# Kernel tuning notes

Hardware: AMD Instinct MI355X
Metric: run time of the kernel (lower is better)

The kernel has to match this reference:

```python
import jax, jax.numpy as jnp
import numpy as np

D_K = 64


def setup_inputs() -> dict:
    key = jax.random.key(0)
    kq, kk, kv, km = jax.random.split(key, 4)
    B, H, S = 4, 16, 2048
    Q = jax.random.normal(kq, (B, H, S, D_K), dtype=jnp.float32)
    K = jax.random.normal(kk, (B, H, S, D_K), dtype=jnp.float32)
    V = jax.random.normal(kv, (B, H, S, D_K), dtype=jnp.float32)
    # boolean mask, True = masked out; broadcast over heads
    mask = jax.random.randint(km, (B, 1, S, S), 0, 2).astype(jnp.bool_)
    return {"Q": Q, "K": K, "V": V, "mask": mask}


def reference(Q, K, V, mask):
    scale = jnp.sqrt(jnp.asarray(D_K, dtype=Q.dtype))
    # [B,H,S,S] scores
    scores = jnp.einsum('bhqd,bhkd->bhqk', Q, K) / scale
    scores = jnp.where(mask, jnp.asarray(-1e9, dtype=scores.dtype), scores)
    attn = jax.nn.softmax(scores, axis=-1)
    return jnp.einsum('bhqk,bhkd->bhqd', attn, V)
```

## Files before the change

### kernel.cpp

```cpp
#include <hip/hip_runtime.h>
#include <hip/hip_bf16.h>


#define SEQ   2048
#define DK    64
#define NB_   4
#define NBH   64
#define KVB   64
#define QB    128
#define NT    (SEQ / KVB)

#define MASKH_WORDS ((size_t)NB_ * SEQ * 64)
#define WSK_OFF ((size_t)2 * 1024 * 1024)
#define WSV_OFF ((size_t)18 * 1024 * 1024)
#define WS_NEED ((size_t)34 * 1024 * 1024)

typedef float    f32x16 __attribute__((ext_vector_type(16)));
typedef _Float16 f16x8  __attribute__((ext_vector_type(8)));
typedef _Float16 f16x2v __attribute__((ext_vector_type(2)));

#define QSCALE 0.18033688011112042f

#if __has_builtin(__builtin_amdgcn_exp2f)
#define EXP2F(x) __builtin_amdgcn_exp2f(x)
#else
__device__ __forceinline__ float EXP2F(float x) {
  float r;
  asm("v_exp_f32 %0, %1\n\ts_nop 1" : "=v"(r) : "v"(x));
  return r;
}
#endif

__device__ __forceinline__ unsigned pkrtz(float lo, float hi) {
  auto v = __builtin_amdgcn_cvt_pkrtz(lo, hi);
  return __builtin_bit_cast(unsigned, v);
}

__device__ __forceinline__ float mzero(float v, unsigned mw, int idx) {
  int s = ((int)(mw << (31 - idx))) >> 31;
  unsigned r = __builtin_bit_cast(unsigned, v) & ~(unsigned)s;
  return __builtin_bit_cast(float, r);
}

#define GLOAD16(g, l)                                                          \
  __builtin_amdgcn_global_load_lds(                                            \
      (const __attribute__((address_space(1))) unsigned*)(g),                  \
      (__attribute__((address_space(3))) unsigned*)(l), 16, 0, 0)

#define BARRIER()                                          \
  do {                                                     \
    asm volatile("s_waitcnt lgkmcnt(0)" ::: "memory");     \
    __builtin_amdgcn_s_barrier();                          \
  } while (0)

__device__ __forceinline__ void halfswap(unsigned a, unsigned b,
                                         unsigned& out_lo, unsigned& out_hi, int hiL) {
#if __has_builtin(__builtin_amdgcn_permlane32_swap)
  auto r = __builtin_amdgcn_permlane32_swap(a, b, false, false);
  out_lo = r[0];
  out_hi = r[1];
#else
  unsigned ax = __shfl_xor(a, 32), bx = __shfl_xor(b, 32);
  out_lo = hiL ? bx : a;
  out_hi = hiL ? b : ax;
#endif
}

__global__ __launch_bounds__(256) void pre_all(
    const int* __restrict__ M, const float* __restrict__ K,
    const float* __restrict__ V, unsigned* __restrict__ Mh,
    _Float16* __restrict__ wsK, _Float16* __restrict__ wsV) {
  const int blk = blockIdx.x;
  if (blk < 2048) {
    int t  = blk * 256 + threadIdx.x;
    int hi = t & 1, T = (t >> 1) & 31, q = (t >> 6) & 2047, b = t >> 17;
    const int* src = M + ((size_t)b * SEQ + q) * SEQ + T * 64 + 4 * hi;
    unsigned bits = 0;
#pragma unroll
    for (int kvb = 0; kvb < 2; ++kvb)
#pragma unroll
      for (int m = 0; m < 4; ++m) {
        int4 v = *(const int4*)(src + 32 * kvb + 8 * m);
        int sh = 16 * kvb + 4 * m;
        bits |= ((unsigned)(v.x != 0) << sh) | ((unsigned)(v.y != 0) << (sh + 1)) |
                ((unsigned)(v.z != 0) << (sh + 2)) | ((unsigned)(v.w != 0) << (sh + 3));
      }
    Mh[t] = bits;
  } else if (blk < 6144) {
    int t  = (blk - 2048) * 256 + threadIdx.x;
    int lq = t & 31, c = (t >> 5) & 15, kt = (t >> 9) & 31, bh = t >> 14;
    int kv = kt * 64 + (c >> 3) * 32 + lq;
    int d0 = ((c >> 1) & 3) * 16 + (c & 1) * 8;
    const float4* src = (const float4*)(K + ((size_t)bh * SEQ + kv) * DK + d0);
    float4 a = src[0], b4 = src[1];
    uint4 o = { pkrtz(a.x, a.y), pkrtz(a.z, a.w), pkrtz(b4.x, b4.y), pkrtz(b4.z, b4.w) };
    *(uint4*)(wsK + (size_t)t * 8) = o;
  } else {
    int t  = (blk - 6144) * 256 + threadIdx.x;
    int lq = t & 31, c = (t >> 5) & 15, kt = (t >> 9) & 31, bh = t >> 14;
    int kv0 = kt * 64 + ((c >> 1) & 3) * 16 + (c & 1) * 8;
    int d   = (c >> 3) * 32 + lq;
    const float* vp = V + ((size_t)bh * SEQ + kv0) * DK + d;
    float v[8];
#pragma unroll
    for (int j = 0; j < 8; ++j) v[j] = vp[(size_t)j * DK];
    uint4 o = { pkrtz(v[0], v[1]), pkrtz(v[2], v[3]), pkrtz(v[4], v[5]), pkrtz(v[6], v[7]) };
    *(uint4*)(wsV + (size_t)t * 8) = o;
  }
}


__global__ __launch_bounds__(256) void sda_attn_pc(
    const float* __restrict__ Q, const unsigned* __restrict__ Mh,
    const _Float16* __restrict__ wsK, const _Float16* __restrict__ wsV,
    float* __restrict__ O) {
  __shared__ __align__(16) _Float16 Kl[2][16 * 256];
  __shared__ __align__(16) _Float16 Vt[3][16 * 256];

  const int bh   = blockIdx.x;
  const int qt   = blockIdx.y;
  const int b    = bh >> 4;
  const int tid  = threadIdx.x;
  const int wid  = tid >> 6;
  const int lane = tid & 63;
  const int lq   = lane & 31;
  const int hiL  = lane >> 5;

  const size_t base = (size_t)bh * SEQ * DK;
  const int    q    = qt * QB + wid * 32 + lq;

  f16x8 qf[4];
  {
    const float* qp = Q + base + (size_t)q * DK + hiL * 8;
#pragma unroll
    for (int kk = 0; kk < 4; ++kk) {
      float4 A  = *(const float4*)(qp + kk * 16);
      float4 Bv = *(const float4*)(qp + kk * 16 + 4);
      uint4 u;
      u.x = pkrtz(A.x * QSCALE, A.y * QSCALE);
      u.y = pkrtz(A.z * QSCALE, A.w * QSCALE);
      u.z = pkrtz(Bv.x * QSCALE, Bv.y * QSCALE);
      u.w = pkrtz(Bv.z * QSCALE, Bv.w * QSCALE);
      qf[kk] = __builtin_bit_cast(f16x8, u);
    }
  }

  f32x16 oacc[2];
#pragma unroll
  for (int db = 0; db < 2; ++db)
#pragma unroll
    for (int r = 0; r < 16; ++r) oacc[db][r] = 0.f;
  float lreg = 0.f;

  const _Float16* skb = wsK + (size_t)bh * 32 * 4096 + wid * 1024 + lane * 8;
  const _Float16* svb = wsV + (size_t)bh * 32 * 4096 + wid * 1024 + lane * 8;
  const unsigned* Mhp = Mh + ((size_t)b * SEQ + q) * 64 + hiL;
  const f16x2v ones = {(_Float16)1.0f, (_Float16)1.0f};
  (void)ones;

#define STAGE2(j_)                                            \
  {                                                           \
    const _Float16* sk = skb + (size_t)(j_) * 4096;           \
    const _Float16* sv = svb + (size_t)(j_) * 4096;           \
    _Float16* dk = &Kl[(j_) & 1][wid * 1024];                 \
    _Float16* dv = &Vt[(j_) % 3][wid * 1024];                 \
    GLOAD16(sk, dk); GLOAD16(sk + 512, dk + 512);             \
    GLOAD16(sv, dv); GLOAD16(sv + 512, dv + 512);             \
  }

#define QKSTEP(SCN, par_)                                                         \
  {                                                                               \
    _Pragma("unroll") for (int kvb = 0; kvb < 2; ++kvb)                           \
      _Pragma("unroll") for (int r = 0; r < 16; ++r) SCN[kvb][r] = 0.f;           \
    __builtin_amdgcn_s_setprio(1);                                                \
    _Pragma("unroll") for (int kk = 0; kk < 4; ++kk)                              \
      _Pragma("unroll") for (int kvb = 0; kvb < 2; ++kvb) {                       \
        f16x8 kf = *(const f16x8*)&Kl[par_][(kvb * 8 + kk * 2 + hiL) * 256 + lq * 8]; \
        SCN[kvb] = __builtin_amdgcn_mfma_f32_32x32x16_f16(kf, qf[kk], SCN[kvb], 0, 0, 0); \
      }                                                                           \
    __builtin_amdgcn_s_setprio(0);                                                \
  }

#define ITER(T_, SCC, SCN, MWV)                                                   \
  {                                                                               \
    const int t_ = (T_);                                                          \
    if (t_ + 2 < NT) STAGE2(t_ + 2);                                              \
    unsigned mwt = (t_ + 2 < NT) ? Mhp[2 * (t_ + 2)] : 0u;                        \
    if (t_ + 1 < NT) QKSTEP(SCN, (t_ + 1) & 1);                                   \
    unsigned pr[2][4][2];                                                         \
    {                                                                             \
      float rs0 = 0.f, rs1 = 0.f;                                                 \
      _Pragma("unroll") for (int kvb = 0; kvb < 2; ++kvb)                         \
        _Pragma("unroll") for (int m = 0; m < 4; ++m) {                           \
          float e0 = mzero(EXP2F(SCC[kvb][4 * m + 0]), MWV, 16 * kvb + 4 * m + 0);\
          float e1 = mzero(EXP2F(SCC[kvb][4 * m + 1]), MWV, 16 * kvb + 4 * m + 1);\
          float e2 = mzero(EXP2F(SCC[kvb][4 * m + 2]), MWV, 16 * kvb + 4 * m + 2);\
          float e3 = mzero(EXP2F(SCC[kvb][4 * m + 3]), MWV, 16 * kvb + 4 * m + 3);\
          unsigned w0 = pkrtz(e0, e1), w1 = pkrtz(e2, e3);                        \
          pr[kvb][m][0] = w0; pr[kvb][m][1] = w1;                                 \
          rs0 += e0 + e1;  rs1 += e2 + e3;                                        \
        }                                                                         \
      float rs = rs0 + rs1;                                                       \
      unsigned ru = __builtin_bit_cast(unsigned, rs), plo, phi;                   \
      halfswap(ru, ru, plo, phi, hiL);                                            \
      lreg += rs + __builtin_bit_cast(float, hiL ? plo : phi);                    \
    }                                                                             \
    _Pragma("unroll") for (int ks = 0; ks < 4; ++ks) {                            \
      const int kvb = ks >> 1, ms = (ks & 1) * 2;                                 \
      unsigned w0, w1, w2, w3;                                                    \
      halfswap(pr[kvb][ms][0], pr[kvb][ms + 1][0], w0, w2, hiL);                  \
      halfswap(pr[kvb][ms][1], pr[kvb][ms + 1][1], w1, w3, hiL);                  \
      f16x8 pf = __builtin_bit_cast(f16x8, make_uint4(w0, w1, w2, w3));           \
      __builtin_amdgcn_s_setprio(1);                                              \
      _Pragma("unroll") for (int db = 0; db < 2; ++db) {                          \
        f16x8 vf = *(const f16x8*)&Vt[t_ % 3][(db * 8 + ks * 2 + hiL) * 256 + lq * 8]; \
        oacc[db] = __builtin_amdgcn_mfma_f32_32x32x16_f16(vf, pf, oacc[db], 0, 0, 0); \
      }                                                                           \
      __builtin_amdgcn_s_setprio(0);                                              \
    }                                                                             \
    MWV = mwt;                                                                    \
    if (t_ + 1 < NT) {                                                            \
      asm volatile("s_waitcnt vmcnt(0)" ::: "memory");                            \
      BARRIER();                                                                  \
    }                                                                             \
  }

  STAGE2(0);
  STAGE2(1);
  unsigned mwA = Mhp[0], mwB = Mhp[2];
  asm volatile("s_waitcnt vmcnt(0)" ::: "memory");
  BARRIER();

  f32x16 scA[2], scB[2];
  QKSTEP(scA, 0);
  BARRIER();

  for (int tt = 0; tt < NT; tt += 2) {
    ITER(tt,     scA, scB, mwA);
    ITER(tt + 1, scB, scA, mwB);
  }

  float inv = (lreg > 0.f) ? 1.0f / lreg : 0.f;
  float* op = O + base + (size_t)q * DK + 4 * hiL;
#pragma unroll
  for (int db = 0; db < 2; ++db)
#pragma unroll
    for (int m = 0; m < 4; ++m) {
      float4 o;
      o.x = oacc[db][4 * m + 0] * inv;
      o.y = oacc[db][4 * m + 1] * inv;
      o.z = oacc[db][4 * m + 2] * inv;
      o.w = oacc[db][4 * m + 3] * inv;
      *(float4*)(op + 32 * db + 8 * m) = o;
    }
}


#define CH 264
__global__ __launch_bounds__(256) void sda_attn_fb(
    const float* __restrict__ Q, const float* __restrict__ K,
    const float* __restrict__ V, const int* __restrict__ M,
    float* __restrict__ O) {
  __shared__ __align__(16) _Float16 Klf[2][16 * CH];
  __shared__ __align__(16) _Float16 Vtf[2][16 * CH];
  const int bh = blockIdx.x, qt = blockIdx.y, b = bh >> 4;
  const int tid = threadIdx.x, wid = tid >> 6, lane = tid & 63;
  const int lq = lane & 31, hiL = lane >> 5;
  const size_t base = (size_t)bh * SEQ * DK;
  const int q = qt * QB + wid * 32 + lq;

  f16x8 qf[4];
  {
    const float* qp = Q + base + (size_t)q * DK + hiL * 8;
#pragma unroll
    for (int kk = 0; kk < 4; ++kk) {
      float4 A = *(const float4*)(qp + kk * 16), Bv = *(const float4*)(qp + kk * 16 + 4);
      uint4 u = { pkrtz(A.x * QSCALE, A.y * QSCALE), pkrtz(A.z * QSCALE, A.w * QSCALE),
                  pkrtz(Bv.x * QSCALE, Bv.y * QSCALE), pkrtz(Bv.z * QSCALE, Bv.w * QSCALE) };
      qf[kk] = __builtin_bit_cast(f16x8, u);
    }
  }
  f32x16 oacc[2];
#pragma unroll
  for (int db = 0; db < 2; ++db)
#pragma unroll
    for (int r = 0; r < 16; ++r) oacc[db][r] = 0.f;
  float lreg = 0.f;

  const int krow = tid >> 2, c0 = tid & 3, kp = tid & 31, d8 = (tid >> 5) * 8;
  const float* Kg = K + base + (size_t)krow * DK + c0 * 16;
  const float* Vg0 = V + base + (size_t)(2 * kp) * DK + d8;
  const float* Vg1 = Vg0 + DK;
  const int kwa = ((krow >> 5) * 8 + c0 * 2) * CH + (krow & 31) * 8;
  const int kwb = kwa + CH;
  const int vwb = ((d8 >> 5) * 8 + (kp >> 3) * 2 + ((kp >> 2) & 1)) * CH +
                  (d8 & 31) * 8 + (kp & 3) * 2;
  float4 kpre[4], vpre[4];
#define FLOADT(kb_)                                                      \
  {                                                                      \
    const float* kg = Kg + (size_t)(kb_)*DK;                             \
    _Pragma("unroll") for (int i = 0; i < 4; ++i)                        \
        kpre[i] = *(const float4*)(kg + 4 * i);                          \
    const float* va = Vg0 + (size_t)(kb_)*DK;                            \
    const float* vb = Vg1 + (size_t)(kb_)*DK;                            \
    vpre[0] = *(const float4*)va; vpre[1] = *(const float4*)(va + 4);    \
    vpre[2] = *(const float4*)vb; vpre[3] = *(const float4*)(vb + 4);    \
  }
#define FSTAGE(b_)                                                          \
  {                                                                         \
    uint4 u0, u1;                                                           \
    u0.x = pkrtz(kpre[0].x, kpre[0].y); u0.y = pkrtz(kpre[0].z, kpre[0].w); \
    u0.z = pkrtz(kpre[1].x, kpre[1].y); u0.w = pkrtz(kpre[1].z, kpre[1].w); \
    u1.x = pkrtz(kpre[2].x, kpre[2].y); u1.y = pkrtz(kpre[2].z, kpre[2].w); \
    u1.z = pkrtz(kpre[3].x, kpre[3].y); u1.w = pkrtz(kpre[3].z, kpre[3].w); \
    *(uint4*)&Klf[b_][kwa] = u0;                                            \
    *(uint4*)&Klf[b_][kwb] = u1;                                            \
    const float* va_ = (const float*)&vpre[0];                              \
    const float* vc_ = (const float*)&vpre[2];                              \
    _Pragma("unroll") for (int j = 0; j < 8; ++j)                           \
        *(unsigned*)&Vtf[b_][vwb + j * 8] = pkrtz(va_[j], vc_[j]);          \
  }
  const int* Mrow = M + ((size_t)b * SEQ + q) * SEQ + 4 * hiL;
  FLOADT(0); FSTAGE(0); FLOADT(KVB);
  BARRIER();
  for (int t = 0; t < NT; ++t) {
    const int cur = t & 1;
    f32x16 sc[2];
#pragma unroll
    for (int kvb = 0; kvb < 2; ++kvb)
#pragma unroll
      for (int r = 0; r < 16; ++r) sc[kvb][r] = 0.f;
#pragma unroll
    for (int kk = 0; kk < 4; ++kk)
#pragma unroll
      for (int kvb = 0; kvb < 2; ++kvb) {
        f16x8 kf = *(const f16x8*)&Klf[cur][(kvb * 8 + kk * 2 + hiL) * CH + lq * 8];
        sc[kvb] = __builtin_amdgcn_mfma_f32_32x32x16_f16(kf, qf[kk], sc[kvb], 0, 0, 0);
      }
    const bool more = (t + 1 < NT);
    if (more) { FSTAGE(cur ^ 1); if (t + 2 < NT) FLOADT((t + 2) * KVB); }
    int4 mraw[8];
#pragma unroll
    for (int kvb = 0; kvb < 2; ++kvb)
#pragma unroll
      for (int m = 0; m < 4; ++m)
        mraw[kvb * 4 + m] = *(const int4*)(Mrow + t * KVB + 32 * kvb + 8 * m);
    float rs = 0.f;
    unsigned pr[2][4][2];
#pragma unroll
    for (int kvb = 0; kvb < 2; ++kvb) {
      float e[16];
#pragma unroll
      for (int r = 0; r < 16; ++r) {
        float ev = EXP2F(sc[kvb][r]);
        int4 v = mraw[kvb * 4 + (r >> 2)];
        int mm = (r & 3) == 0 ? v.x : (r & 3) == 1 ? v.y : (r & 3) == 2 ? v.z : v.w;
        ev = mm != 0 ? 0.f : ev;
        e[r] = ev; rs += ev;
      }
#pragma unroll
      for (int m = 0; m < 4; ++m) {
        pr[kvb][m][0] = pkrtz(e[4 * m + 0], e[4 * m + 1]);
        pr[kvb][m][1] = pkrtz(e[4 * m + 2], e[4 * m + 3]);
      }
    }
    {
      unsigned ru = __builtin_bit_cast(unsigned, rs), plo, phi;
      halfswap(ru, ru, plo, phi, hiL);
      lreg += rs + __builtin_bit_cast(float, hiL ? plo : phi);
    }
#pragma unroll
    for (int ks = 0; ks < 4; ++ks) {
      const int kvb = ks >> 1, ms = (ks & 1) * 2;
      unsigned w0, w1, w2, w3;
      halfswap(pr[kvb][ms][0], pr[kvb][ms + 1][0], w0, w2, hiL);
      halfswap(pr[kvb][ms][1], pr[kvb][ms + 1][1], w1, w3, hiL);
      f16x8 pf = __builtin_bit_cast(f16x8, make_uint4(w0, w1, w2, w3));
#pragma unroll
      for (int db = 0; db < 2; ++db) {
        f16x8 vf = *(const f16x8*)&Vtf[cur][(db * 8 + ks * 2 + hiL) * CH + lq * 8];
        oacc[db] = __builtin_amdgcn_mfma_f32_32x32x16_f16(vf, pf, oacc[db], 0, 0, 0);
      }
    }
    if (more) BARRIER();
  }
  float inv = (lreg > 0.f) ? 1.0f / lreg : 0.f;
  float* op = O + base + (size_t)q * DK + 4 * hiL;
#pragma unroll
  for (int db = 0; db < 2; ++db)
#pragma unroll
    for (int m = 0; m < 4; ++m) {
      float4 o;
      o.x = oacc[db][4 * m + 0] * inv;
      o.y = oacc[db][4 * m + 1] * inv;
      o.z = oacc[db][4 * m + 2] * inv;
      o.w = oacc[db][4 * m + 3] * inv;
      *(float4*)(op + 32 * db + 8 * m) = o;
    }
}

extern "C" void kernel_launch(void* const* d_in, const int* in_sizes, int n_in,
                              void* d_out, int out_size, void* d_ws, size_t ws_size,
                              hipStream_t stream) {
  const float* Q = (const float*)d_in[0];
  const float* K = (const float*)d_in[1];
  const float* V = (const float*)d_in[2];
  const int*   M = (const int*)d_in[3];
  float*       O = (float*)d_out;
  dim3 grid(NBH, SEQ / QB);

  if (ws_size >= WS_NEED) {
    unsigned*  Mh  = (unsigned*)d_ws;
    _Float16*  wsK = (_Float16*)((char*)d_ws + WSK_OFF);
    _Float16*  wsV = (_Float16*)((char*)d_ws + WSV_OFF);
    pre_all<<<10240, 256, 0, stream>>>(M, K, V, Mh, wsK, wsV);
    sda_attn_pc<<<grid, 256, 0, stream>>>(Q, Mh, wsK, wsV, O);
  } else {
    sda_attn_fb<<<grid, 256, 0, stream>>>(Q, K, V, M, O);
  }
}
```

Before: 144.6 us.

## Expand mask to per-lane fp16 AND-masks and simplify pipeline to double buffering

The preprocessing kernel now stores the mask as per-lane 16-bit AND masks (64 bytes per lane per tile) in the MFMA fragment order, in place of packed bits. The attention loop applies them with a bitwise AND on the packed fp16 probabilities and computes row sums with fdot2. This replaces the per-element shift/mask ops and float adds. The software pipeline drops the lookahead QK step and triple-buffered V in favour of simple double buffering. The trade-off is 16x more mask traffic (32 MB workspace read per pass), less overlap between QK and PV across iterations, and fp16-accumulated row-sum inputs.

```diff
diff --git a/kernel.cpp b/kernel.cpp
--- a/kernel.cpp
+++ b/kernel.cpp
@@ -10,10 +10,9 @@
 #define QB    128
 #define NT    (SEQ / KVB)
 
-#define MASKH_WORDS ((size_t)NB_ * SEQ * 64)
-#define WSK_OFF ((size_t)2 * 1024 * 1024)
-#define WSV_OFF ((size_t)18 * 1024 * 1024)
-#define WS_NEED ((size_t)34 * 1024 * 1024)
+#define WSK_OFF ((size_t)32 * 1024 * 1024)
+#define WSV_OFF ((size_t)48 * 1024 * 1024)
+#define WS_NEED ((size_t)64 * 1024 * 1024)
 
 typedef float    f32x16 __attribute__((ext_vector_type(16)));
 typedef _Float16 f16x8  __attribute__((ext_vector_type(8)));
@@ -34,12 +33,6 @@
 __device__ __forceinline__ unsigned pkrtz(float lo, float hi) {
   auto v = __builtin_amdgcn_cvt_pkrtz(lo, hi);
   return __builtin_bit_cast(unsigned, v);
-}
-
-__device__ __forceinline__ float mzero(float v, unsigned mw, int idx) {
-  int s = ((int)(mw << (31 - idx))) >> 31;
-  unsigned r = __builtin_bit_cast(unsigned, v) & ~(unsigned)s;
-  return __builtin_bit_cast(float, r);
 }
 
 #define GLOAD16(g, l)                                                          \
@@ -68,24 +61,31 @@
 
 __global__ __launch_bounds__(256) void pre_all(
     const int* __restrict__ M, const float* __restrict__ K,
-    const float* __restrict__ V, unsigned* __restrict__ Mh,
+    const float* __restrict__ V, uint4* __restrict__ Mx,
     _Float16* __restrict__ wsK, _Float16* __restrict__ wsV) {
   const int blk = blockIdx.x;
   if (blk < 2048) {
-    int t  = blk * 256 + threadIdx.x;
-    int hi = t & 1, T = (t >> 1) & 31, q = (t >> 6) & 2047, b = t >> 17;
-    const int* src = M + ((size_t)b * SEQ + q) * SEQ + T * 64 + 4 * hi;
-    unsigned bits = 0;
+    int t_id = blk * 256 + threadIdx.x;
+    int lane = t_id & 63, t = (t_id >> 6) & 31, wid = (t_id >> 11) & 3;
+    int qt = (t_id >> 13) & 15, b = t_id >> 17;
+    int hiL = lane >> 5, lq = lane & 31;
+    int q = qt * QB + wid * 32 + lq;
+    const int* mrow = M + ((size_t)b * SEQ + q) * SEQ;
+    unsigned w[16];
 #pragma unroll
     for (int kvb = 0; kvb < 2; ++kvb)
 #pragma unroll
       for (int m = 0; m < 4; ++m) {
-        int4 v = *(const int4*)(src + 32 * kvb + 8 * m);
-        int sh = 16 * kvb + 4 * m;
-        bits |= ((unsigned)(v.x != 0) << sh) | ((unsigned)(v.y != 0) << (sh + 1)) |
-                ((unsigned)(v.z != 0) << (sh + 2)) | ((unsigned)(v.w != 0) << (sh + 3));
+        int kv = t * 64 + kvb * 32 + 8 * m + 4 * hiL;
+        int4 v = *(const int4*)(mrow + kv);
+        w[kvb * 8 + 2 * m + 0] = (v.x ? 0u : 0xFFFFu) | (v.y ? 0u : 0xFFFF0000u);
+        w[kvb * 8 + 2 * m + 1] = (v.z ? 0u : 0xFFFFu) | (v.w ? 0u : 0xFFFF0000u);
       }
-    Mh[t] = bits;
+    uint4* dst = Mx + (size_t)t_id * 4;
+    dst[0] = make_uint4(w[0], w[1], w[2], w[3]);
+    dst[1] = make_uint4(w[4], w[5], w[6], w[7]);
+    dst[2] = make_uint4(w[8], w[9], w[10], w[11]);
+    dst[3] = make_uint4(w[12], w[13], w[14], w[15]);
   } else if (blk < 6144) {
     int t  = (blk - 2048) * 256 + threadIdx.x;
     int lq = t & 31, c = (t >> 5) & 15, kt = (t >> 9) & 31, bh = t >> 14;
@@ -111,11 +111,11 @@
 
 
 __global__ __launch_bounds__(256) void sda_attn_pc(
-    const float* __restrict__ Q, const unsigned* __restrict__ Mh,
+    const float* __restrict__ Q, const uint4* __restrict__ Mx,
     const _Float16* __restrict__ wsK, const _Float16* __restrict__ wsV,
     float* __restrict__ O) {
   __shared__ __align__(16) _Float16 Kl[2][16 * 256];
-  __shared__ __align__(16) _Float16 Vt[3][16 * 256];
+  __shared__ __align__(16) _Float16 Vt[2][16 * 256];
 
   const int bh   = blockIdx.x;
   const int qt   = blockIdx.y;
@@ -154,52 +154,59 @@
 
   const _Float16* skb = wsK + (size_t)bh * 32 * 4096 + wid * 1024 + lane * 8;
   const _Float16* svb = wsV + (size_t)bh * 32 * 4096 + wid * 1024 + lane * 8;
-  const unsigned* Mhp = Mh + ((size_t)b * SEQ + q) * 64 + hiL;
+  const uint4* Mx0 = Mx + ((size_t)(((b * 16 + qt) * 4 + wid) * 32) * 64 + lane) * 4;
+
+#define STAGE_GL(buf_, kt_)                                   \
+  {                                                           \
+    const _Float16* sk = skb + (size_t)(kt_) * 4096;          \
+    const _Float16* sv = svb + (size_t)(kt_) * 4096;          \
+    _Float16* dk = &Kl[buf_][wid * 1024];                     \
+    _Float16* dv = &Vt[buf_][wid * 1024];                     \
+    GLOAD16(sk, dk); GLOAD16(sk + 512, dk + 512);             \
+    GLOAD16(sv, dv); GLOAD16(sv + 512, dv + 512);             \
+  }
+
   const f16x2v ones = {(_Float16)1.0f, (_Float16)1.0f};
   (void)ones;
 
-#define STAGE2(j_)                                            \
-  {                                                           \
-    const _Float16* sk = skb + (size_t)(j_) * 4096;           \
-    const _Float16* sv = svb + (size_t)(j_) * 4096;           \
-    _Float16* dk = &Kl[(j_) & 1][wid * 1024];                 \
-    _Float16* dv = &Vt[(j_) % 3][wid * 1024];                 \
-    GLOAD16(sk, dk); GLOAD16(sk + 512, dk + 512);             \
-    GLOAD16(sv, dv); GLOAD16(sv + 512, dv + 512);             \
-  }
-
-#define QKSTEP(SCN, par_)                                                         \
+#define ITER(T_, MA, MB)                                                          \
   {                                                                               \
+    const int t_ = (T_);                                                          \
+    const int cur_ = t_ & 1;                                                      \
+    const bool more_ = (t_ + 1 < NT);                                             \
+    if (more_) {                                                                  \
+      STAGE_GL(cur_ ^ 1, t_ + 1);                                                 \
+      const uint4* mp_ = Mx0 + (size_t)(t_ + 1) * 256;                            \
+      MB[0] = mp_[0]; MB[1] = mp_[1]; MB[2] = mp_[2]; MB[3] = mp_[3];             \
+    }                                                                             \
+    f32x16 sc[2];                                                                 \
     _Pragma("unroll") for (int kvb = 0; kvb < 2; ++kvb)                           \
-      _Pragma("unroll") for (int r = 0; r < 16; ++r) SCN[kvb][r] = 0.f;           \
+      _Pragma("unroll") for (int r = 0; r < 16; ++r) sc[kvb][r] = 0.f;            \
     __builtin_amdgcn_s_setprio(1);                                                \
     _Pragma("unroll") for (int kk = 0; kk < 4; ++kk)                              \
       _Pragma("unroll") for (int kvb = 0; kvb < 2; ++kvb) {                       \
-        f16x8 kf = *(const f16x8*)&Kl[par_][(kvb * 8 + kk * 2 + hiL) * 256 + lq * 8]; \
-        SCN[kvb] = __builtin_amdgcn_mfma_f32_32x32x16_f16(kf, qf[kk], SCN[kvb], 0, 0, 0); \
+        f16x8 kf = *(const f16x8*)&Kl[cur_][(kvb * 8 + kk * 2 + hiL) * 256 + lq * 8]; \
+        sc[kvb] = __builtin_amdgcn_mfma_f32_32x32x16_f16(kf, qf[kk], sc[kvb], 0, 0, 0); \
       }                                                                           \
     __builtin_amdgcn_s_setprio(0);                                                \
-  }
-
-#define ITER(T_, SCC, SCN, MWV)                                                   \
-  {                                                                               \
-    const int t_ = (T_);                                                          \
-    if (t_ + 2 < NT) STAGE2(t_ + 2);                                              \
-    unsigned mwt = (t_ + 2 < NT) ? Mhp[2 * (t_ + 2)] : 0u;                        \
-    if (t_ + 1 < NT) QKSTEP(SCN, (t_ + 1) & 1);                                   \
+    float rs0 = 0.f, rs1 = 0.f;                                                   \
     unsigned pr[2][4][2];                                                         \
+    _Pragma("unroll") for (int kvb = 0; kvb < 2; ++kvb)                           \
+      _Pragma("unroll") for (int m = 0; m < 4; ++m) {                             \
+        float e0 = EXP2F(sc[kvb][4 * m + 0]);                                     \
+        float e1 = EXP2F(sc[kvb][4 * m + 1]);                                     \
+        float e2 = EXP2F(sc[kvb][4 * m + 2]);                                     \
+        float e3 = EXP2F(sc[kvb][4 * m + 3]);                                     \
+        const int j0 = kvb * 8 + 2 * m;                                           \
+        unsigned mw0 = ((const unsigned*)&MA[j0 >> 2])[j0 & 3];                   \
+        unsigned mw1 = ((const unsigned*)&MA[(j0 + 1) >> 2])[(j0 + 1) & 3];       \
+        unsigned w0 = pkrtz(e0, e1) & mw0;                                        \
+        unsigned w1 = pkrtz(e2, e3) & mw1;                                        \
+        pr[kvb][m][0] = w0; pr[kvb][m][1] = w1;                                   \
+        rs0 = __builtin_amdgcn_fdot2(__builtin_bit_cast(f16x2v, w0), ones, rs0, false); \
+        rs1 = __builtin_amdgcn_fdot2(__builtin_bit_cast(f16x2v, w1), ones, rs1, false); \
+      }                                                                           \
     {                                                                             \
-      float rs0 = 0.f, rs1 = 0.f;                                                 \
-      _Pragma("unroll") for (int kvb = 0; kvb < 2; ++kvb)                         \
-        _Pragma("unroll") for (int m = 0; m < 4; ++m) {                           \
-          float e0 = mzero(EXP2F(SCC[kvb][4 * m + 0]), MWV, 16 * kvb + 4 * m + 0);\
-          float e1 = mzero(EXP2F(SCC[kvb][4 * m + 1]), MWV, 16 * kvb + 4 * m + 1);\
-          float e2 = mzero(EXP2F(SCC[kvb][4 * m + 2]), MWV, 16 * kvb + 4 * m + 2);\
-          float e3 = mzero(EXP2F(SCC[kvb][4 * m + 3]), MWV, 16 * kvb + 4 * m + 3);\
-          unsigned w0 = pkrtz(e0, e1), w1 = pkrtz(e2, e3);                        \
-          pr[kvb][m][0] = w0; pr[kvb][m][1] = w1;                                 \
-          rs0 += e0 + e1;  rs1 += e2 + e3;                                        \
-        }                                                                         \
       float rs = rs0 + rs1;                                                       \
       unsigned ru = __builtin_bit_cast(unsigned, rs), plo, phi;                   \
       halfswap(ru, ru, plo, phi, hiL);                                            \
@@ -213,31 +220,26 @@
       f16x8 pf = __builtin_bit_cast(f16x8, make_uint4(w0, w1, w2, w3));           \
       __builtin_amdgcn_s_setprio(1);                                              \
       _Pragma("unroll") for (int db = 0; db < 2; ++db) {                          \
-        f16x8 vf = *(const f16x8*)&Vt[t_ % 3][(db * 8 + ks * 2 + hiL) * 256 + lq * 8]; \
+        f16x8 vf = *(const f16x8*)&Vt[cur_][(db * 8 + ks * 2 + hiL) * 256 + lq * 8]; \
         oacc[db] = __builtin_amdgcn_mfma_f32_32x32x16_f16(vf, pf, oacc[db], 0, 0, 0); \
       }                                                                           \
       __builtin_amdgcn_s_setprio(0);                                              \
     }                                                                             \
-    MWV = mwt;                                                                    \
-    if (t_ + 1 < NT) {                                                            \
+    if (more_) {                                                                  \
       asm volatile("s_waitcnt vmcnt(0)" ::: "memory");                            \
       BARRIER();                                                                  \
     }                                                                             \
   }
 
-  STAGE2(0);
-  STAGE2(1);
-  unsigned mwA = Mhp[0], mwB = Mhp[2];
+  uint4 ma[4], mb[4];
+  STAGE_GL(0, 0);
+  ma[0] = Mx0[0]; ma[1] = Mx0[1]; ma[2] = Mx0[2]; ma[3] = Mx0[3];
   asm volatile("s_waitcnt vmcnt(0)" ::: "memory");
   BARRIER();
 
-  f32x16 scA[2], scB[2];
-  QKSTEP(scA, 0);
-  BARRIER();
-
   for (int tt = 0; tt < NT; tt += 2) {
-    ITER(tt,     scA, scB, mwA);
-    ITER(tt + 1, scB, scA, mwB);
+    ITER(tt,     ma, mb);
+    ITER(tt + 1, mb, ma);
   }
 
   float inv = (lreg > 0.f) ? 1.0f / lreg : 0.f;
@@ -410,11 +412,11 @@
   dim3 grid(NBH, SEQ / QB);
 
   if (ws_size >= WS_NEED) {
-    unsigned*  Mh  = (unsigned*)d_ws;
+    uint4*     Mx  = (uint4*)d_ws;
     _Float16*  wsK = (_Float16*)((char*)d_ws + WSK_OFF);
     _Float16*  wsV = (_Float16*)((char*)d_ws + WSV_OFF);
-    pre_all<<<10240, 256, 0, stream>>>(M, K, V, Mh, wsK, wsV);
-    sda_attn_pc<<<grid, 256, 0, stream>>>(Q, Mh, wsK, wsV, O);
+    pre_all<<<10240, 256, 0, stream>>>(M, K, V, Mx, wsK, wsV);
+    sda_attn_pc<<<grid, 256, 0, stream>>>(Q, Mx, wsK, wsV, O);
   } else {
     sda_attn_fb<<<grid, 256, 0, stream>>>(Q, K, V, M, O);
   }
```

Result: no change. 147.2 us (+1.8%).
